# Performance work log

Hardware: AMD Instinct MI355X
Metric: run time of the kernel (lower is better)

Reference implementation:

```python
import jax, jax.numpy as jnp
import numpy as np
from jax import lax

B, NP = 4, 8192          # events, points per event (equal-sized batches)
RATIO, R, K = 0.25, 0.2, 64
MP = int(NP * RATIO)     # sampled centers per event
D_IN = 32
BIG = 1e10


def _fps_one(pos):
    # Farthest point sampling (deterministic start at index 0). pos: [NP,3] -> [MP] int32
    d = jnp.sum((pos - pos[0]) ** 2, axis=-1)
    sel = jnp.zeros((MP,), jnp.int32)

    def body(i, carry):
        sel, d = carry
        nxt = jnp.argmax(d).astype(jnp.int32)
        sel = sel.at[i].set(nxt)
        d = jnp.minimum(d, jnp.sum((pos - pos[nxt]) ** 2, axis=-1))
        return sel, d

    sel, _ = lax.fori_loop(1, MP, body, (sel, d))
    return sel


def _ball_query_one(centers, pos):
    # centers: [MP,3], pos: [NP,3] -> neighbor idx [MP,K] int32, validity mask [MP,K]
    d2 = jnp.sum((centers[:, None, :] - pos[None, :, :]) ** 2, axis=-1)  # [MP,NP]
    d2m = jnp.where(d2 <= R * R, d2, BIG)
    neg, idx = lax.top_k(-d2m, K)          # K nearest within radius (deterministic)
    mask = (-neg) <= R * R
    return idx.astype(jnp.int32), mask


def reference(x, pos, batch, W1, b1, W2, b2, W3, b3):
    xb = x.reshape(B, NP, D_IN)
    pb = pos.reshape(B, NP, 3)

    sel = jax.vmap(_fps_one)(pb)                                   # [B,MP]
    centers = jnp.take_along_axis(pb, sel[..., None], axis=1)      # [B,MP,3]
    idx, mask = jax.vmap(_ball_query_one)(centers, pb)             # [B,MP,K]

    gather = jax.vmap(lambda a, i: a[i])
    pos_j = gather(pb, idx)                                        # [B,MP,K,3]
    x_j = gather(xb, idx)                                          # [B,MP,K,D_IN]

    rel = pos_j - centers[:, :, None, :]
    h = jnp.concatenate([x_j, rel], axis=-1)                       # [B,MP,K,D_IN+3]
    h = jax.nn.relu(h @ W1 + b1)
    h = jax.nn.relu(h @ W2 + b2)
    h = jax.nn.relu(h @ W3 + b3)                                   # [B,MP,K,128]

    h = jnp.where(mask[..., None], h, -BIG)
    x_out = jnp.max(h, axis=2).reshape(B * MP, -1)                 # max aggregation
    pos_out = centers.reshape(B * MP, 3)
    batch_out = jnp.repeat(jnp.arange(B, dtype=jnp.int32), MP)
    return x_out, pos_out, batch_out


def setup_inputs() -> dict:
    key = jax.random.key(0)
    ks = jax.random.split(key, 8)
    x = jax.random.normal(ks[0], (B * NP, D_IN), jnp.float32)
    pos = jax.random.uniform(ks[1], (B * NP, 3), jnp.float32)
    batch = (jnp.arange(B * NP) // NP).astype(jnp.int64)
    W1 = jax.random.normal(ks[2], (D_IN + 3, 64), jnp.float32) * 0.05
    b1 = jnp.zeros((64,), jnp.float32)
    W2 = jax.random.normal(ks[3], (64, 64), jnp.float32) * 0.05
    b2 = jnp.zeros((64,), jnp.float32)
    W3 = jax.random.normal(ks[4], (64, 128), jnp.float32) * 0.05
    b3 = jnp.zeros((128,), jnp.float32)
    return {"x": x, "pos": pos, "batch": batch, "W1": W1, "b1": b1,
            "W2": W2, "b2": b2, "W3": W3, "b3": b3}
```

## Files before the change

kernel.cpp:

```cpp
#include <hip/hip_runtime.h>


#define BATCH 4
#define NP 8192
#define MP 2048
#define KNN 64
#define DIN 32
#define NWORK 200
#define NBLK (BATCH + NWORK)
#define CAND_CAP 512

#define DPP_FMAX(v, ctrl)                                                     \
  {                                                                           \
    int _t = __builtin_amdgcn_update_dpp(__float_as_int(v),                   \
                                         __float_as_int(v), (ctrl), 0xF,      \
                                         0xF, false);                         \
    (v) = fmaxf((v), __int_as_float(_t));                                     \
  }

#define DPP_MINU(v, ctrl)                                                     \
  {                                                                           \
    unsigned _t = (unsigned)__builtin_amdgcn_update_dpp((int)(v), (int)(v),   \
                                                        (ctrl), 0xF, 0xF,    \
                                                        false);               \
    (v) = ((v) < _t) ? (v) : _t;                                              \
  }

#define DPP_WAVEMAX6(v)                                                       \
  {                                                                           \
    DPP_FMAX(v, 0x111); DPP_FMAX(v, 0x112); DPP_FMAX(v, 0x114);               \
    DPP_FMAX(v, 0x118); DPP_FMAX(v, 0x142); DPP_FMAX(v, 0x143);               \
  }

#define DPP_WAVEMINU6(v)                                                      \
  {                                                                           \
    DPP_MINU(v, 0x111); DPP_MINU(v, 0x112); DPP_MINU(v, 0x114);               \
    DPP_MINU(v, 0x118); DPP_MINU(v, 0x142); DPP_MINU(v, 0x143);               \
  }

typedef float v2f __attribute__((ext_vector_type(2)));

__device__ __forceinline__ int aload(const int* p) {
  return __hip_atomic_load(p, __ATOMIC_RELAXED, __HIP_MEMORY_SCOPE_AGENT);
}
__device__ __forceinline__ void astore_i(int* p, int v) {
  __hip_atomic_store(p, v, __ATOMIC_RELAXED, __HIP_MEMORY_SCOPE_AGENT);
}
__device__ __forceinline__ float afload(const float* p) {
  return __hip_atomic_load(p, __ATOMIC_RELAXED, __HIP_MEMORY_SCOPE_AGENT);
}
__device__ __forceinline__ void afstore(float* p, float v) {
  __hip_atomic_store(p, v, __ATOMIC_RELAXED, __HIP_MEMORY_SCOPE_AGENT);
}

__global__ void init_k(int* __restrict__ flags) {
  if (threadIdx.x < 8) flags[threadIdx.x] = 0;
}

__global__ __launch_bounds__(1024) void mega_k(const float* __restrict__ pos,
                                               const float* __restrict__ x,
                                               const float* __restrict__ W1,
                                               const float* __restrict__ b1,
                                               const float* __restrict__ W2,
                                               const float* __restrict__ b2,
                                               const float* __restrict__ W3,
                                               const float* __restrict__ b3,
                                               float* __restrict__ pout,
                                               float* __restrict__ bout,
                                               float* __restrict__ P1,
                                               float* __restrict__ W2T,
                                               float* __restrict__ xout,
                                               int* __restrict__ flags)
{
  __shared__ __align__(16) float smem[NP * 3];
  __shared__ unsigned long long slt[2][16];

  int* const prog   = flags;
  int* const ticket = flags + 4;
  int* const p1done = flags + 5;

  const int bid = blockIdx.x;
  const int tid = threadIdx.x;
  const int lane = tid & 63, wid = tid >> 6;

  if (bid < BATCH) {
    const int b = bid;
    float* const ptab = smem;
    const float* __restrict__ pb = pos + (size_t)b * NP * 3;
    const int base = tid * 8;

    bout[b * MP + tid] = (float)b;
    bout[b * MP + 1024 + tid] = (float)b;

    float t[24];
    const float4* __restrict__ pv = (const float4*)(pb + (size_t)tid * 24);
#pragma unroll
    for (int q = 0; q < 6; q++) *(float4*)&t[q * 4] = pv[q];
#pragma unroll
    for (int q = 0; q < 6; q++)
      *(float4*)&ptab[tid * 24 + q * 4] = *(float4*)&t[q * 4];

    v2f px[4], py[4], pz[4], d[4];
#pragma unroll
    for (int j = 0; j < 4; j++) {
      px[j].x = t[6 * j + 0]; py[j].x = t[6 * j + 1]; pz[j].x = t[6 * j + 2];
      px[j].y = t[6 * j + 3]; py[j].y = t[6 * j + 4]; pz[j].y = t[6 * j + 5];
    }

    const float c0x = pb[0], c0y = pb[1], c0z = pb[2];
    if (tid == 0) {
      afstore(&pout[(size_t)b * MP * 3 + 0], c0x);
      afstore(&pout[(size_t)b * MP * 3 + 1], c0y);
      afstore(&pout[(size_t)b * MP * 3 + 2], c0z);
    }

    float bv = -1.f;
    {
      v2f cx = {c0x, c0x}, cy = {c0y, c0y}, cz = {c0z, c0z};
#pragma unroll
      for (int j = 0; j < 4; j++) {
        v2f dx = px[j] - cx, dy = py[j] - cy, dz = pz[j] - cz;
        v2f nd = dx * dx + dy * dy + dz * dz;
        d[j] = nd;
        bv = fmaxf(bv, fmaxf(nd.x, nd.y));
      }
    }

    for (int i = 1; i < MP; i++) {
      float v = bv;
      DPP_WAVEMAX6(v);
      const float wmax =
          __int_as_float(__builtin_amdgcn_readlane(__float_as_int(v), 63));

      const unsigned long long m = __ballot(bv == wmax);
      const int src = (int)__builtin_ctzll(m);
      const int p = i & 1;
      if (lane == src) {
        int ks = 7;
#pragma unroll
        for (int k = 6; k >= 0; k--) {
          float dv = (k & 1) ? d[k >> 1].y : d[k >> 1].x;
          if (dv == wmax) ks = k;
        }
        slt[p][wid] = ((unsigned long long)__float_as_uint(wmax) << 32)
                      | (unsigned)(base + ks);
      }
      __syncthreads();

      const unsigned long long kv = slt[p][lane & 15];
      const float v2 = __uint_as_float((unsigned)(kv >> 32));
      float v2r = v2;
      DPP_FMAX(v2r, 0x111);
      DPP_FMAX(v2r, 0x112);
      DPP_FMAX(v2r, 0x114);
      DPP_FMAX(v2r, 0x118);
      const float mv =
          __int_as_float(__builtin_amdgcn_readlane(__float_as_int(v2r), 15));
      const unsigned long long m2 = __ballot(v2 == mv);
      const int mw = (int)__builtin_ctzll(m2);
      const int js = __builtin_amdgcn_readlane((int)(unsigned)kv, mw);
      const float ncx = ptab[js * 3 + 0];
      const float ncy = ptab[js * 3 + 1];
      const float ncz = ptab[js * 3 + 2];

      if (tid == 0) {
        afstore(&pout[((size_t)b * MP + i) * 3 + 0], ncx);
        afstore(&pout[((size_t)b * MP + i) * 3 + 1], ncy);
        afstore(&pout[((size_t)b * MP + i) * 3 + 2], ncz);
        if ((i & 15) == 15) {
          asm volatile("s_waitcnt vmcnt(0)" ::: "memory");
          astore_i(&prog[b], i + 1);
        }
      }

      const v2f cx = {ncx, ncx}, cy = {ncy, ncy}, cz = {ncz, ncz};
      bv = -1.f;
#pragma unroll
      for (int j = 0; j < 4; j++) {
        v2f dx = px[j] - cx, dy = py[j] - cy, dz = pz[j] - cz;
        v2f nd = dx * dx + dy * dy + dz * dz;
        v2f dn;
        dn.x = fminf(d[j].x, nd.x);
        dn.y = fminf(d[j].y, nd.y);
        d[j] = dn;
        bv = fmaxf(bv, fmaxf(dn.x, dn.y));
      }
    }
    return;
  }

  {
    const int wbid = bid - BATCH;
    for (size_t e = (size_t)wbid * 1024 + tid; e < (size_t)32768 * 64;
         e += (size_t)NWORK * 1024) {
      const int j = (int)(e >> 6), c = (int)(e & 63);
      const float* __restrict__ xr = x + (size_t)j * DIN;
      float acc = 0.f;
#pragma unroll
      for (int k = 0; k < DIN; k++) acc += xr[k] * W1[k * 64 + c];
      P1[(size_t)j * 64 + c] = acc;
    }
    if (bid == BATCH) {
      for (int e = tid; e < 64 * 64; e += 1024) {
        const int c = e >> 6, k = e & 63;
        W2T[e] = W2[k * 64 + c];
      }
    }
    __syncthreads();
    if (tid == 0) { __threadfence(); atomicAdd(p1done, 1); }
  }

  unsigned long long* const cw =
      (unsigned long long*)smem + (size_t)wid * CAND_CAP;
  const float R2 = (float)(0.2 * 0.2);
  bool mlp_ready = false;

  for (;;) {
    int t;
    if (lane == 0) t = atomicAdd(ticket, 1);
    t = __builtin_amdgcn_readfirstlane(t);
    if (t >= BATCH * MP) break;
    const int b = t & 3;
    const int cIdx = t >> 2;
    const int wg = b * MP + cIdx;

    while (aload(&prog[b]) < cIdx + 1) __builtin_amdgcn_s_sleep(32);
    const float cx = afload(&pout[(size_t)wg * 3 + 0]);
    const float cy = afload(&pout[(size_t)wg * 3 + 1]);
    const float cz = afload(&pout[(size_t)wg * 3 + 2]);

    const float* __restrict__ pb = pos + (size_t)b * NP * 3;

    int cnt = 0;
    for (int basej = 0; basej < NP; basej += 64) {
      const int j = basej + lane;
      float dx = pb[j * 3 + 0] - cx;
      float dy = pb[j * 3 + 1] - cy;
      float dz = pb[j * 3 + 2] - cz;
      float d2 = dx * dx + dy * dy + dz * dz;
      bool in = (d2 <= R2);
      unsigned long long mb = __ballot(in);
      int pre = (int)__popcll(mb & ((1ull << lane) - 1ull));
      int slot = cnt + pre;
      if (in && slot < CAND_CAP)
        cw[slot] = ((unsigned long long)__float_as_uint(d2) << 32)
                   | (unsigned int)j;
      cnt += (int)__popcll(mb);
    }
    if (cnt > CAND_CAP) cnt = CAND_CAP;

    unsigned long long last = 0;
    int myout = -1;
    for (int r = 0; r < KNN; r++) {
      unsigned long long v = ~0ull;
      for (int s = lane; s < cnt; s += 64) {
        const unsigned long long c = cw[s];
        if (c >= last && c < v) v = c;
      }
      const unsigned hi = (unsigned)(v >> 32);
      unsigned h = hi;
      DPP_WAVEMINU6(h);
      const unsigned mhi = (unsigned)__builtin_amdgcn_readlane((int)h, 63);
      const unsigned lo = (hi == mhi) ? (unsigned)v : 0xffffffffu;
      unsigned l2 = lo;
      DPP_WAVEMINU6(l2);
      const unsigned mlo = (unsigned)__builtin_amdgcn_readlane((int)l2, 63);
      if (lane == r) myout = (mhi == 0xffffffffu) ? -1 : (int)mlo;
      last = (mhi == 0xffffffffu)
                 ? ~0ull
                 : ((((unsigned long long)mhi << 32) | mlo) + 1ull);
    }

    if (!mlp_ready) {
      while (aload(p1done) < NWORK) __builtin_amdgcn_s_sleep(32);
      __threadfence();
      mlp_ready = true;
    }

    const int idx = myout;
    const bool valid = idx >= 0;
    const int j = valid ? idx : 0;
    const float* __restrict__ pj = pos + ((size_t)b * NP + j) * 3;
    const float rx = pj[0] - cx, ry = pj[1] - cy, rz = pj[2] - cz;
    const float* __restrict__ p1r = (const float*)__builtin_assume_aligned(
        P1 + ((size_t)b * NP + j) * 64, 16);

    float h1[64];
#pragma unroll
    for (int k = 0; k < 64; k++) {
      float vv = p1r[k] + rx * W1[32 * 64 + k] + ry * W1[33 * 64 + k]
                        + rz * W1[34 * 64 + k] + b1[k];
      h1[k] = fmaxf(vv, 0.f);
    }

    float4 keep = make_float4(0.f, 0.f, 0.f, 0.f);
    for (int pass = 0; pass < 4; pass++) {
      float acc[32];
#pragma unroll
      for (int g = 0; g < 32; g++) acc[g] = b3[pass * 32 + g];
#pragma unroll 2
      for (int c = 0; c < 64; c++) {
        const float* __restrict__ w = W2T + c * 64;
        float a0 = 0.f, a1 = 0.f, a2 = 0.f, a3 = 0.f;
#pragma unroll
        for (int k4 = 0; k4 < 16; k4++) {
          a0 += h1[k4 * 4 + 0] * w[k4 * 4 + 0];
          a1 += h1[k4 * 4 + 1] * w[k4 * 4 + 1];
          a2 += h1[k4 * 4 + 2] * w[k4 * 4 + 2];
          a3 += h1[k4 * 4 + 3] * w[k4 * 4 + 3];
        }
        const float h2c = fmaxf(b2[c] + ((a0 + a1) + (a2 + a3)), 0.f);
        const float* __restrict__ w3r = W3 + c * 128 + pass * 32;
#pragma unroll
        for (int g = 0; g < 32; g++) acc[g] += h2c * w3r[g];
      }
#pragma unroll
      for (int g4 = 0; g4 < 8; g4++) {
        float a0 = valid ? fmaxf(acc[g4 * 4 + 0], 0.f) : 0.f;
        float a1 = valid ? fmaxf(acc[g4 * 4 + 1], 0.f) : 0.f;
        float a2 = valid ? fmaxf(acc[g4 * 4 + 2], 0.f) : 0.f;
        float a3 = valid ? fmaxf(acc[g4 * 4 + 3], 0.f) : 0.f;
        DPP_WAVEMAX6(a0);
        DPP_WAVEMAX6(a1);
        DPP_WAVEMAX6(a2);
        DPP_WAVEMAX6(a3);
        const float m0 =
            __int_as_float(__builtin_amdgcn_readlane(__float_as_int(a0), 63));
        const float m1 =
            __int_as_float(__builtin_amdgcn_readlane(__float_as_int(a1), 63));
        const float m2 =
            __int_as_float(__builtin_amdgcn_readlane(__float_as_int(a2), 63));
        const float m3 =
            __int_as_float(__builtin_amdgcn_readlane(__float_as_int(a3), 63));
        if (lane == pass * 8 + g4) {
          keep.x = m0; keep.y = m1; keep.z = m2; keep.w = m3;
        }
      }
    }
    if (lane < 32)
      *(float4*)&xout[(size_t)wg * 128 + lane * 4] = keep;
  }
}

extern "C" void kernel_launch(void* const* d_in, const int* in_sizes, int n_in,
                              void* d_out, int out_size, void* d_ws, size_t ws_size,
                              hipStream_t stream)
{
  const float* x   = (const float*)d_in[0];
  const float* pos = (const float*)d_in[1];
  const float* W1 = (const float*)d_in[3];
  const float* b1 = (const float*)d_in[4];
  const float* W2 = (const float*)d_in[5];
  const float* b2 = (const float*)d_in[6];
  const float* W3 = (const float*)d_in[7];
  const float* b3 = (const float*)d_in[8];

  float* out  = (float*)d_out;
  float* xout = out;
  float* pout = out + 8192 * 128;
  float* bout = out + 8192 * 128 + 8192 * 3;

  char* ws = (char*)d_ws;
  float* P1    = (float*)ws;
  float* W2T   = (float*)(ws + 8388608);
  int*   flags = (int*)(ws + 8404992);

  init_k<<<dim3(1), dim3(64), 0, stream>>>(flags);
  mega_k<<<dim3(NBLK), dim3(1024), 0, stream>>>(pos, x, W1, b1, W2, b2, W3,
                                                b3, pout, bout, P1, W2T,
                                                xout, flags);
}
```

Measured before the change: 2.447 ms.

## Fuse first-layer projection into per-neighbor MLP and shard workers per batch

Drops the P1 precompute phase (x·W1 over all points) and the W2 transpose, and instead computes the x·W1 product per neighbor inline in the MLP lane, reading W2 directly. Worker blocks are halved and each is pinned to one batch with its own ticket counter and progress flag on separate cache lines. Polling uses an adaptive sleep that waits longer when far behind the FPS producer. This removes a global barrier and the P1 round trip, but does redundant x·W1 work for points that appear in several neighborhoods, adds register pressure, and uses strided W2 reads.

```diff
diff --git a/kernel.cpp b/kernel.cpp
--- a/kernel.cpp
+++ b/kernel.cpp
@@ -6,7 +6,7 @@
 #define MP 2048
 #define KNN 64
 #define DIN 32
-#define NWORK 200
+#define NWORK 100
 #define NBLK (BATCH + NWORK)
 #define CAND_CAP 512
 
@@ -54,7 +54,7 @@
 }
 
 __global__ void init_k(int* __restrict__ flags) {
-  if (threadIdx.x < 8) flags[threadIdx.x] = 0;
+  flags[threadIdx.x] = 0;
 }
 
 __global__ __launch_bounds__(1024) void mega_k(const float* __restrict__ pos,
@@ -67,24 +67,19 @@
                                                const float* __restrict__ b3,
                                                float* __restrict__ pout,
                                                float* __restrict__ bout,
-                                               float* __restrict__ P1,
-                                               float* __restrict__ W2T,
                                                float* __restrict__ xout,
                                                int* __restrict__ flags)
 {
   __shared__ __align__(16) float smem[NP * 3];
   __shared__ unsigned long long slt[2][16];
 
-  int* const prog   = flags;
-  int* const ticket = flags + 4;
-  int* const p1done = flags + 5;
-
   const int bid = blockIdx.x;
   const int tid = threadIdx.x;
   const int lane = tid & 63, wid = tid >> 6;
 
   if (bid < BATCH) {
     const int b = bid;
+    int* const prog = &flags[b * 32];
     float* const ptab = smem;
     const float* __restrict__ pb = pos + (size_t)b * NP * 3;
     const int base = tid * 8;
@@ -169,7 +164,7 @@
         afstore(&pout[((size_t)b * MP + i) * 3 + 2], ncz);
         if ((i & 15) == 15) {
           asm volatile("s_waitcnt vmcnt(0)" ::: "memory");
-          astore_i(&prog[b], i + 1);
+          astore_i(prog, i + 1);
         }
       }
 
@@ -189,47 +184,30 @@
     return;
   }
 
-  {
-    const int wbid = bid - BATCH;
-    for (size_t e = (size_t)wbid * 1024 + tid; e < (size_t)32768 * 64;
-         e += (size_t)NWORK * 1024) {
-      const int j = (int)(e >> 6), c = (int)(e & 63);
-      const float* __restrict__ xr = x + (size_t)j * DIN;
-      float acc = 0.f;
-#pragma unroll
-      for (int k = 0; k < DIN; k++) acc += xr[k] * W1[k * 64 + c];
-      P1[(size_t)j * 64 + c] = acc;
-    }
-    if (bid == BATCH) {
-      for (int e = tid; e < 64 * 64; e += 1024) {
-        const int c = e >> 6, k = e & 63;
-        W2T[e] = W2[k * 64 + c];
-      }
-    }
-    __syncthreads();
-    if (tid == 0) { __threadfence(); atomicAdd(p1done, 1); }
-  }
-
+  const int b = (bid - BATCH) & 3;
+  int* const prog = &flags[b * 32];
+  int* const tk   = &flags[128 + b * 32];
   unsigned long long* const cw =
       (unsigned long long*)smem + (size_t)wid * CAND_CAP;
   const float R2 = (float)(0.2 * 0.2);
-  bool mlp_ready = false;
+  const float* __restrict__ pb = pos + (size_t)b * NP * 3;
 
   for (;;) {
     int t;
-    if (lane == 0) t = atomicAdd(ticket, 1);
+    if (lane == 0) t = atomicAdd(tk, 1);
     t = __builtin_amdgcn_readfirstlane(t);
-    if (t >= BATCH * MP) break;
-    const int b = t & 3;
-    const int cIdx = t >> 2;
+    if (t >= MP) break;
+    const int cIdx = t;
     const int wg = b * MP + cIdx;
 
-    while (aload(&prog[b]) < cIdx + 1) __builtin_amdgcn_s_sleep(32);
+    int pr;
+    while ((pr = aload(prog)) < cIdx + 1) {
+      if (cIdx + 1 - pr > 64) __builtin_amdgcn_s_sleep(127);
+      else                    __builtin_amdgcn_s_sleep(8);
+    }
     const float cx = afload(&pout[(size_t)wg * 3 + 0]);
     const float cy = afload(&pout[(size_t)wg * 3 + 1]);
     const float cz = afload(&pout[(size_t)wg * 3 + 2]);
-
-    const float* __restrict__ pb = pos + (size_t)b * NP * 3;
 
     int cnt = 0;
     for (int basej = 0; basej < NP; basej += 64) {
@@ -271,25 +249,36 @@
                  : ((((unsigned long long)mhi << 32) | mlo) + 1ull);
     }
 
-    if (!mlp_ready) {
-      while (aload(p1done) < NWORK) __builtin_amdgcn_s_sleep(32);
-      __threadfence();
-      mlp_ready = true;
-    }
-
     const int idx = myout;
     const bool valid = idx >= 0;
     const int j = valid ? idx : 0;
     const float* __restrict__ pj = pos + ((size_t)b * NP + j) * 3;
     const float rx = pj[0] - cx, ry = pj[1] - cy, rz = pj[2] - cz;
-    const float* __restrict__ p1r = (const float*)__builtin_assume_aligned(
-        P1 + ((size_t)b * NP + j) * 64, 16);
 
     float h1[64];
 #pragma unroll
+    for (int k = 0; k < 64; k++) h1[k] = 0.f;
+    {
+      const float* __restrict__ xr = x + ((size_t)b * NP + j) * DIN;
+#pragma unroll
+      for (int half = 0; half < 2; half++) {
+        float xv[16];
+#pragma unroll
+        for (int q = 0; q < 4; q++)
+          *(float4*)&xv[q * 4] = ((const float4*)xr)[half * 4 + q];
+#pragma unroll
+        for (int c = 0; c < 16; c++) {
+          const float xc = xv[c];
+          const float* __restrict__ w = W1 + (half * 16 + c) * 64;
+#pragma unroll
+          for (int k = 0; k < 64; k++) h1[k] += xc * w[k];
+        }
+      }
+    }
+#pragma unroll
     for (int k = 0; k < 64; k++) {
-      float vv = p1r[k] + rx * W1[32 * 64 + k] + ry * W1[33 * 64 + k]
-                        + rz * W1[34 * 64 + k] + b1[k];
+      float vv = h1[k] + rx * W1[32 * 64 + k] + ry * W1[33 * 64 + k]
+                       + rz * W1[34 * 64 + k] + b1[k];
       h1[k] = fmaxf(vv, 0.f);
     }
 
@@ -300,14 +289,13 @@
       for (int g = 0; g < 32; g++) acc[g] = b3[pass * 32 + g];
 #pragma unroll 2
       for (int c = 0; c < 64; c++) {
-        const float* __restrict__ w = W2T + c * 64;
         float a0 = 0.f, a1 = 0.f, a2 = 0.f, a3 = 0.f;
 #pragma unroll
         for (int k4 = 0; k4 < 16; k4++) {
-          a0 += h1[k4 * 4 + 0] * w[k4 * 4 + 0];
-          a1 += h1[k4 * 4 + 1] * w[k4 * 4 + 1];
-          a2 += h1[k4 * 4 + 2] * w[k4 * 4 + 2];
-          a3 += h1[k4 * 4 + 3] * w[k4 * 4 + 3];
+          a0 += h1[k4 * 4 + 0] * W2[(k4 * 4 + 0) * 64 + c];
+          a1 += h1[k4 * 4 + 1] * W2[(k4 * 4 + 1) * 64 + c];
+          a2 += h1[k4 * 4 + 2] * W2[(k4 * 4 + 2) * 64 + c];
+          a3 += h1[k4 * 4 + 3] * W2[(k4 * 4 + 3) * 64 + c];
         }
         const float h2c = fmaxf(b2[c] + ((a0 + a1) + (a2 + a3)), 0.f);
         const float* __restrict__ w3r = W3 + c * 128 + pass * 32;
@@ -360,13 +348,9 @@
   float* pout = out + 8192 * 128;
   float* bout = out + 8192 * 128 + 8192 * 3;
 
-  char* ws = (char*)d_ws;
-  float* P1    = (float*)ws;
-  float* W2T   = (float*)(ws + 8388608);
-  int*   flags = (int*)(ws + 8404992);
-
-  init_k<<<dim3(1), dim3(64), 0, stream>>>(flags);
+  int* flags = (int*)d_ws;
+
+  init_k<<<dim3(1), dim3(256), 0, stream>>>(flags);
   mega_k<<<dim3(NBLK), dim3(1024), 0, stream>>>(pos, x, W1, b1, W2, b2, W3,
-                                                b3, pout, bout, P1, W2T,
-                                                xout, flags);
-}
+                                                b3, pout, bout, xout, flags);
+}
```

Result: faster. 2.290 ms (-6.4%).
